# Optimization experiments

Hardware: AMD Instinct MI355X
Metric: run time of the kernel (lower is better)

The kernel has to match this reference:

```python
import jax, jax.numpy as jnp
import numpy as np
import math

D_MODEL = 1024
N_HEADS = 16
D_K = D_MODEL // N_HEADS


def setup_inputs() -> dict:
    key = jax.random.key(0)
    ks = jax.random.split(key, 9)
    s = 1.0 / math.sqrt(D_MODEL)
    x = jax.random.normal(ks[0], (2, 2048, D_MODEL), dtype=jnp.float32)
    # nn.Linear stores weight as [out, in]; we store transposed [in, out] for x @ W
    Wq = jax.random.uniform(ks[1], (D_MODEL, D_MODEL), jnp.float32, -s, s)
    bq = jax.random.uniform(ks[2], (D_MODEL,), jnp.float32, -s, s)
    Wk = jax.random.uniform(ks[3], (D_MODEL, D_MODEL), jnp.float32, -s, s)
    bk = jax.random.uniform(ks[4], (D_MODEL,), jnp.float32, -s, s)
    Wv = jax.random.uniform(ks[5], (D_MODEL, D_MODEL), jnp.float32, -s, s)
    bv = jax.random.uniform(ks[6], (D_MODEL,), jnp.float32, -s, s)
    Wo = jax.random.uniform(ks[7], (D_MODEL, D_MODEL), jnp.float32, -s, s)
    bo = jax.random.uniform(ks[8], (D_MODEL,), jnp.float32, -s, s)
    return {"x": x, "Wq": Wq, "bq": bq, "Wk": Wk, "bk": bk,
            "Wv": Wv, "bv": bv, "Wo": Wo, "bo": bo}


def reference(x, Wq, bq, Wk, bk, Wv, bv, Wo, bo):
    B, S, _ = x.shape
    scale = 1.0 / math.sqrt(D_K)
    # projections -> [B, H, S, Dk]
    def split_heads(t):
        return t.reshape(B, S, N_HEADS, D_K).transpose(0, 2, 1, 3)
    q = split_heads(x @ Wq + bq)
    k = split_heads(x @ Wk + bk)
    v = split_heads(x @ Wv + bv)
    # [B, H, S, S] scores
    scores = jnp.einsum('bhqd,bhkd->bhqk', q, k) * scale
    weights = jax.nn.softmax(scores, axis=-1)  # dropout p=0.0 -> identity
    attn = jnp.einsum('bhqk,bhkd->bhqd', weights, v)
    attn = attn.transpose(0, 2, 1, 3).reshape(B, S, D_MODEL)
    return attn @ Wo + bo
```

## Files before the change

### kernel.cpp

```cpp
#include <hip/hip_runtime.h>

#define DM    1024
#define NTOK  4096

typedef __attribute__((ext_vector_type(8))) short short8;
typedef __attribute__((ext_vector_type(4))) float floatx4;

__device__ __forceinline__ ushort f2bf(float f) {
  union { float f; uint32_t u; } v; v.f = f;
  uint32_t r = (v.u + 0x7fffu + ((v.u >> 16) & 1u)) >> 16;
  return (ushort)r;
}
__device__ __forceinline__ uint f2bf2(float a, float b) {
  return (uint)f2bf(a) | ((uint)f2bf(b) << 16);
}
__device__ __forceinline__ uint pkhi(float a, float b) {
  uint ua = __float_as_uint(a) + 0x8000u;
  uint ub = __float_as_uint(b) + 0x8000u;
  return __builtin_amdgcn_perm(ub, ua, 0x07060302);
}

__device__ __forceinline__ floatx4 mfma16(short8 a, short8 b, floatx4 c) {
  return __builtin_amdgcn_mfma_f32_16x16x32_bf16(a, b, c, 0, 0, 0);
}

__device__ __forceinline__ void glld16(const ushort* g, ushort* l) {
  __builtin_amdgcn_global_load_lds(
      (const __attribute__((address_space(1))) void*)g,
      (__attribute__((address_space(3))) void*)l, 16, 0, 0);
}

__device__ __forceinline__ void stage_slab(const ushort* gbase, int strideHW,
                                           ushort* lds, int ii, int lane) {
  const int r = ii * 8 + (lane >> 3);
  const int c = (lane & 7) ^ (r & 7);
  glld16(gbase + (size_t)r * strideHW + c * 8, lds + ii * 512);
}

__device__ __forceinline__ short8 fragr(const ushort* lds, int row, int chunk) {
  return *reinterpret_cast<const short8*>(&lds[row * 64 + ((chunk ^ (row & 7)) << 3)]);
}

__global__ __launch_bounds__(256) void k_prep(const float* __restrict__ x,
                                              const float* __restrict__ Wq,
                                              const float* __restrict__ Wk,
                                              const float* __restrict__ Wv,
                                              const float* __restrict__ Wo,
                                              ushort* __restrict__ xb,
                                              ushort* __restrict__ Wtout) {
  __shared__ ushort T[64 * 72];
  const int bx = blockIdx.x, tid = threadIdx.x;
  if (bx < 2048) {
    int i = (bx * 256 + tid) * 8;
    float4 f0 = *reinterpret_cast<const float4*>(x + i);
    float4 f1 = *reinterpret_cast<const float4*>(x + i + 4);
    short8 o;
    o[0] = (short)f2bf(f0.x); o[1] = (short)f2bf(f0.y);
    o[2] = (short)f2bf(f0.z); o[3] = (short)f2bf(f0.w);
    o[4] = (short)f2bf(f1.x); o[5] = (short)f2bf(f1.y);
    o[6] = (short)f2bf(f1.z); o[7] = (short)f2bf(f1.w);
    *reinterpret_cast<short8*>(xb + i) = o;
    return;
  }
  const int idx = bx - 2048;
  const int z = idx >> 8, rem = idx & 255;
  const float* W = (z == 0) ? Wq : (z == 1) ? Wk : (z == 2) ? Wv : Wo;
  ushort* Wt = Wtout + (size_t)z * (DM * DM);
  const int br = (rem >> 4) * 64;
  const int bc = (rem & 15) * 64;
  const int tr = tid >> 2;
  const int tc = (tid & 3) * 16;

  const float* src = W + (size_t)(br + tr) * DM + bc + tc;
#pragma unroll
  for (int j = 0; j < 4; ++j) {
    float4 v = *reinterpret_cast<const float4*>(src + j * 4);
    T[(tc + j * 4 + 0) * 72 + tr] = f2bf(v.x);
    T[(tc + j * 4 + 1) * 72 + tr] = f2bf(v.y);
    T[(tc + j * 4 + 2) * 72 + tr] = f2bf(v.z);
    T[(tc + j * 4 + 3) * 72 + tr] = f2bf(v.w);
  }
  __syncthreads();
  ushort* dst = Wt + (size_t)(bc + tr) * DM + br + tc;
  *reinterpret_cast<int4*>(dst) = *reinterpret_cast<const int4*>(&T[tr * 72 + tc]);
  *reinterpret_cast<int4*>(dst + 8) = *reinterpret_cast<const int4*>(&T[tr * 72 + tc + 8]);
}

__global__ __launch_bounds__(256) void k_gemm_qkv(const ushort* __restrict__ Am,
                                                  const ushort* __restrict__ Bm,
                                                  const float* __restrict__ bq,
                                                  const float* __restrict__ bk,
                                                  const float* __restrict__ bv,
                                                  ushort* __restrict__ Qo,
                                                  ushort* __restrict__ Ko,
                                                  ushort* __restrict__ Vto) {
  __shared__ ushort smem[32768];
  const int tid = threadIdx.x;
  const int w = tid >> 6, lane = tid & 63;
  const int quad = lane >> 4, l15 = lane & 15;
  const int wm = w >> 1, wn = w & 1;
  const int bm = blockIdx.x & 31, bn = blockIdx.x >> 5;
  const int sel = bn >> 3;
  const int bnl = bn & 7;

  const ushort* Ab = Am + (size_t)bm * 128 * 1024;
  const ushort* Bb = Bm + (size_t)bn * 128 * 1024;

  floatx4 acc[4][4] = {};

  auto stage = [&](int it, int buf) {
    ushort* As = smem + buf * 16384;
    ushort* Bs = As + 8192;
    const int k0 = it * 64;
#pragma unroll
    for (int i = 0; i < 4; ++i) stage_slab(Ab + k0, 1024, As, w * 4 + i, lane);
#pragma unroll
    for (int i = 0; i < 4; ++i) stage_slab(Bb + k0, 1024, Bs, w * 4 + i, lane);
  };

  stage(0, 0);
  for (int it = 0; it < 16; ++it) {
    __syncthreads();
    if (it + 1 < 16) stage(it + 1, (it + 1) & 1);
    const ushort* As = smem + (it & 1) * 16384;
    const ushort* Bs = As + 8192;
#pragma unroll
    for (int ks = 0; ks < 2; ++ks) {
      short8 af[4], bf[4];
#pragma unroll
      for (int t = 0; t < 4; ++t) {
        af[t] = fragr(As, wm * 64 + t * 16 + l15, ks * 4 + quad);
        bf[t] = fragr(Bs, wn * 64 + t * 16 + l15, ks * 4 + quad);
      }
#pragma unroll
      for (int tm = 0; tm < 4; ++tm)
#pragma unroll
        for (int tn = 0; tn < 4; ++tn)
          acc[tm][tn] = mfma16(af[tm], bf[tn], acc[tm][tn]);
    }
  }

  if (sel < 2) {
    const float* bp = sel ? bk : bq;
    ushort* dst = sel ? Ko : Qo;
    const float sc = sel ? 1.0f : 0.18033688f;
#pragma unroll
    for (int tm = 0; tm < 4; ++tm)
#pragma unroll
      for (int tn = 0; tn < 4; ++tn) {
        const int mg0 = bm * 128 + wm * 64 + tm * 16 + quad * 4;
        const int np = bnl * 128 + wn * 64 + tn * 16 + l15;
        const float bb = bp[np];
#pragma unroll
        for (int r = 0; r < 4; ++r) {
          const int m = mg0 + r;
          float v = (acc[tm][tn][r] + bb) * sc;
          dst[(size_t)((m >> 11) * 16 + (np >> 6)) * 131072 + (m & 2047) * 64 + (np & 63)] = f2bf(v);
        }
      }
  } else {
    __syncthreads();
    ushort* T = smem;
#pragma unroll
    for (int tm = 0; tm < 4; ++tm)
#pragma unroll
      for (int tn = 0; tn < 4; ++tn) {
        const int ml = wm * 64 + tm * 16 + quad * 4;
        const int nl = wn * 64 + tn * 16 + l15;
        const float bb = bv[bnl * 128 + nl];
        uint p0 = f2bf2(acc[tm][tn][0] + bb, acc[tm][tn][1] + bb);
        uint p1 = f2bf2(acc[tm][tn][2] + bb, acc[tm][tn][3] + bb);
        *reinterpret_cast<uint*>(&T[nl * 136 + ml]) = p0;
        *reinterpret_cast<uint*>(&T[nl * 136 + ml + 2]) = p1;
      }
    __syncthreads();
    const int tok0 = bm * 128;
    const int b = tok0 >> 11, s0 = tok0 & 2047;
    const int col = (tid & 15) * 8;
#pragma unroll
    for (int i = 0; i < 8; ++i) {
      const int rowl = i * 16 + (tid >> 4);
      const int dp = bnl * 128 + rowl;
      const int h = dp >> 6, d = dp & 63;
      *reinterpret_cast<int4*>(Vto + (size_t)((b * 16 + h) * 64 + d) * 2048 + s0 + col) =
          *reinterpret_cast<int4*>(&T[rowl * 136 + col]);
    }
  }
}

__global__ __launch_bounds__(256) void k_gemm_out(const ushort* __restrict__ Am,
                                                  const ushort* __restrict__ Bm,
                                                  const float* __restrict__ bias,
                                                  float* __restrict__ outp) {
  __shared__ ushort smem[24576];
  const int tid = threadIdx.x;
  const int w = tid >> 6, lane = tid & 63;
  const int quad = lane >> 4, l15 = lane & 15;
  const int wm = w >> 1, wn = w & 1;
  const int bm = blockIdx.x >> 3, bn = blockIdx.x & 7;

  const ushort* Ab = Am + (size_t)bm * 64 * 1024;
  const ushort* Bb = Bm + (size_t)bn * 128 * 1024;

  floatx4 acc[2][4] = {};

  auto stage = [&](int it, int buf) {
    ushort* As = smem + buf * 12288;
    ushort* Bs = As + 4096;
    const int k0 = it * 64;
#pragma unroll
    for (int i = 0; i < 2; ++i) stage_slab(Ab + k0, 1024, As, w * 2 + i, lane);
#pragma unroll
    for (int i = 0; i < 4; ++i) stage_slab(Bb + k0, 1024, Bs, w * 4 + i, lane);
  };

  stage(0, 0);
  for (int it = 0; it < 16; ++it) {
    __syncthreads();
    if (it + 1 < 16) stage(it + 1, (it + 1) & 1);
    const ushort* As = smem + (it & 1) * 12288;
    const ushort* Bs = As + 4096;
#pragma unroll
    for (int ks = 0; ks < 2; ++ks) {
      short8 af[2], bf[4];
#pragma unroll
      for (int t = 0; t < 2; ++t)
        af[t] = fragr(As, wm * 32 + t * 16 + l15, ks * 4 + quad);
#pragma unroll
      for (int t = 0; t < 4; ++t)
        bf[t] = fragr(Bs, wn * 64 + t * 16 + l15, ks * 4 + quad);
#pragma unroll
      for (int tm = 0; tm < 2; ++tm)
#pragma unroll
        for (int tn = 0; tn < 4; ++tn)
          acc[tm][tn] = mfma16(af[tm], bf[tn], acc[tm][tn]);
    }
  }

#pragma unroll
  for (int tm = 0; tm < 2; ++tm)
#pragma unroll
    for (int tn = 0; tn < 4; ++tn) {
      const int mg0 = bm * 64 + wm * 32 + tm * 16 + quad * 4;
      const int ng = bn * 128 + wn * 64 + tn * 16 + l15;
      const float bb = bias[ng];
#pragma unroll
      for (int r = 0; r < 4; ++r)
        outp[(size_t)(mg0 + r) * 1024 + ng] = acc[tm][tn][r] + bb;
    }
}

__global__ __launch_bounds__(256) void k_attn(const ushort* __restrict__ Q,
                                              const ushort* __restrict__ Kc,
                                              const ushort* __restrict__ Vt,
                                              ushort* __restrict__ attnb) {
  __shared__ ushort KV[2][16384];
  const int tid = threadIdx.x;
  const int w = tid >> 6, lane = tid & 63;
  const int quad = lane >> 4, l15 = lane & 15;
  const int bx = blockIdx.x;
  const int bh = (bx & 7) * 4 + ((bx >> 3) & 3);
  const int qc = bx >> 5;
  const int qt0 = qc * 128 + w * 32;
  const ushort* Qb = Q + (size_t)bh * 131072;
  const ushort* Kp = Kc + (size_t)bh * 131072;
  const ushort* Vp = Vt + (size_t)bh * 131072;

  short8 qf[2][2];
#pragma unroll
  for (int qs = 0; qs < 2; ++qs)
#pragma unroll
    for (int ks = 0; ks < 2; ++ks)
      qf[qs][ks] = *reinterpret_cast<const short8*>(
          Qb + (size_t)(qt0 + qs * 16 + l15) * 64 + ks * 32 + quad * 8);

  const int krho8 = lane >> 3;
  const int vt_ = (lane & 7) ^ (lane >> 3);

  auto stage = [&](int kt, int buf) {
#pragma unroll
    for (int i = 0; i < 2; ++i) {
      const int sub = (w & 1) * 2 + i;
      const int kc = kt * 128 + sub * 32;
      if (w < 2) {
        ushort* dst = &KV[buf][sub * 2048];
#pragma unroll
        for (int si = 0; si < 4; ++si) {
          const int rho = si * 8 + krho8;
          const int g = ((rho >> 2) & 3) * 8 + ((rho >> 4) & 1) * 4 + (rho & 3);
          const int cc = (lane & 7) ^ (rho & 7);
          glld16(Kp + (size_t)(kc + g) * 64 + cc * 8, dst + si * 512);
        }
      } else {
        ushort* dst = &KV[buf][8192 + sub * 2048];
#pragma unroll
        for (int si = 0; si < 4; ++si) {
          const int d = (si * 8 + krho8) * 2 + (vt_ >> 2);
          glld16(Vp + (size_t)d * 2048 + kc + (vt_ & 3) * 8, dst + si * 512);
        }
      }
    }
  };

  floatx4 oaccT[2][4] = {};
  floatx4 lacc[2] = {};

  auto computeChunk = [&](const ushort* Kb, const ushort* Vb) {
    floatx4 st[2][2] = {};
#pragma unroll
    for (int ks = 0; ks < 2; ++ks) {
      short8 kf0 = fragr(Kb, l15, ks * 4 + quad);
      short8 kf1 = fragr(Kb, 16 + l15, ks * 4 + quad);
      st[0][0] = mfma16(kf0, qf[0][ks], st[0][0]);
      st[0][1] = mfma16(kf1, qf[0][ks], st[0][1]);
      st[1][0] = mfma16(kf0, qf[1][ks], st[1][0]);
      st[1][1] = mfma16(kf1, qf[1][ks], st[1][1]);
    }
    short8 vf[4];
#pragma unroll
    for (int tn = 0; tn < 4; ++tn) {
      const int pg = tn * 8 + (l15 >> 1);
      const int cc = ((l15 & 1) * 4 + quad) ^ (l15 >> 1);
      vf[tn] = *reinterpret_cast<const short8*>(&Vb[pg * 64 + cc * 8]);
    }
#pragma unroll
    for (int qs = 0; qs < 2; ++qs) {
      floatx4 p0, p1;
#pragma unroll
      for (int r = 0; r < 4; ++r) {
        p0[r] = __builtin_amdgcn_exp2f(st[qs][0][r]);
        p1[r] = __builtin_amdgcn_exp2f(st[qs][1][r]);
      }
      lacc[qs] += p0;
      lacc[qs] += p1;
      union { uint4 u; short8 s; } pb;
      pb.u = (uint4){pkhi(p0[0], p0[1]), pkhi(p0[2], p0[3]),
                     pkhi(p1[0], p1[1]), pkhi(p1[2], p1[3])};
#pragma unroll
      for (int tn = 0; tn < 4; ++tn)
        oaccT[qs][tn] = mfma16(vf[tn], pb.s, oaccT[qs][tn]);
    }
  };

  stage(0, 0);
  for (int kt = 0; kt < 16; ++kt) {
    __syncthreads();
    if (kt + 1 < 16) stage(kt + 1, (kt + 1) & 1);
    const ushort* buf = KV[kt & 1];
#pragma unroll
    for (int c = 0; c < 4; ++c)
      computeChunk(buf + c * 2048, buf + 8192 + c * 2048);
  }

  float linv[2];
#pragma unroll
  for (int qs = 0; qs < 2; ++qs) {
    float l = lacc[qs][0] + lacc[qs][1] + lacc[qs][2] + lacc[qs][3];
    l += __shfl_xor(l, 16);
    l += __shfl_xor(l, 32);
    linv[qs] = 1.0f / l;
  }

  const int b = bh >> 4, h = bh & 15;
#pragma unroll
  for (int qs = 0; qs < 2; ++qs) {
    const int tok = b * 2048 + qt0 + qs * 16 + l15;
#pragma unroll
    for (int tn = 0; tn < 4; ++tn) {
      float v0 = oaccT[qs][tn][0] * linv[qs];
      float v1 = oaccT[qs][tn][1] * linv[qs];
      float v2 = oaccT[qs][tn][2] * linv[qs];
      float v3 = oaccT[qs][tn][3] * linv[qs];
      ushort* p = attnb + (size_t)tok * 1024 + h * 64 + tn * 16 + quad * 4;
      *reinterpret_cast<uint*>(p) = pkhi(v0, v1);
      *reinterpret_cast<uint*>(p + 2) = pkhi(v2, v3);
    }
  }
}

extern "C" void kernel_launch(void* const* d_in, const int* in_sizes, int n_in,
                              void* d_out, int out_size, void* d_ws, size_t ws_size,
                              hipStream_t stream) {
  const float* x  = (const float*)d_in[0];
  const float* Wq = (const float*)d_in[1];
  const float* bq = (const float*)d_in[2];
  const float* Wk = (const float*)d_in[3];
  const float* bk = (const float*)d_in[4];
  const float* Wv = (const float*)d_in[5];
  const float* bv = (const float*)d_in[6];
  const float* Wo = (const float*)d_in[7];
  const float* bo = (const float*)d_in[8];

  ushort* ws = (ushort*)d_ws;
  ushort* xb    = ws;
  ushort* Wqt   = ws + 4194304;
  ushort* Wot   = ws + 7340032;
  ushort* Qb    = ws + 8388608;
  ushort* Kbuf  = ws + 12582912;
  ushort* Vtb   = ws + 16777216;
  ushort* attnb = ws + 20971520;

  k_prep<<<3072, 256, 0, stream>>>(x, Wq, Wk, Wv, Wo, xb, Wqt);
  k_gemm_qkv<<<768, 256, 0, stream>>>(xb, Wqt, bq, bk, bv, Qb, Kbuf, Vtb);
  k_attn<<<512, 256, 0, stream>>>(Qb, Kbuf, Vtb, attnb);
  k_gemm_out<<<512, 256, 0, stream>>>(attnb, Wot, bo, (float*)d_out);
}
```

Baseline: 183.6 us.

## Halve attention KV tile, compute softmax denominator via MFMA, use packed bf16 convert

The attention kernel's shared K/V staging buffer is halved (64 keys per stage instead of 128), doubling the loop count while cutting LDS per block, which may allow more resident blocks. The per-lane fp32 row-sum accumulation and cross-lane shuffles are replaced by an extra MFMA against a vector of bf16 ones, so the denominator comes out of the matrix unit. The probability packing uses the hardware cvt_pk_bf16 instruction when available. The trade-off is more barriers and stage iterations, an extra MFMA per chunk, and a denominator summed from bf16-rounded probabilities.

```diff
diff --git a/kernel.cpp b/kernel.cpp
--- a/kernel.cpp
+++ b/kernel.cpp
@@ -5,6 +5,7 @@
 
 typedef __attribute__((ext_vector_type(8))) short short8;
 typedef __attribute__((ext_vector_type(4))) float floatx4;
+typedef __attribute__((ext_vector_type(2))) __bf16 bf16x2;
 
 __device__ __forceinline__ ushort f2bf(float f) {
   union { float f; uint32_t u; } v; v.f = f;
@@ -18,6 +19,15 @@
   uint ua = __float_as_uint(a) + 0x8000u;
   uint ub = __float_as_uint(b) + 0x8000u;
   return __builtin_amdgcn_perm(ub, ua, 0x07060302);
+}
+__device__ __forceinline__ uint pk2(float a, float b) {
+#if __has_builtin(__builtin_amdgcn_cvt_pk_bf16_f32)
+  bf16x2 v = __builtin_amdgcn_cvt_pk_bf16_f32(a, b);
+  union { bf16x2 v; uint u; } c; c.v = v;
+  return c.u;
+#else
+  return pkhi(a, b);
+#endif
 }
 
 __device__ __forceinline__ floatx4 mfma16(short8 a, short8 b, floatx4 c) {
@@ -254,7 +264,7 @@
                                               const ushort* __restrict__ Kc,
                                               const ushort* __restrict__ Vt,
                                               ushort* __restrict__ attnb) {
-  __shared__ ushort KV[2][16384];
+  __shared__ ushort KV[2][8192];
   const int tid = threadIdx.x;
   const int w = tid >> 6, lane = tid & 63;
   const int quad = lane >> 4, l15 = lane & 15;
@@ -274,36 +284,36 @@
       qf[qs][ks] = *reinterpret_cast<const short8*>(
           Qb + (size_t)(qt0 + qs * 16 + l15) * 64 + ks * 32 + quad * 8);
 
+  short8 ones;
+#pragma unroll
+  for (int i = 0; i < 8; ++i) ones[i] = (short)0x3F80;
+
   const int krho8 = lane >> 3;
   const int vt_ = (lane & 7) ^ (lane >> 3);
 
   auto stage = [&](int kt, int buf) {
-#pragma unroll
-    for (int i = 0; i < 2; ++i) {
-      const int sub = (w & 1) * 2 + i;
-      const int kc = kt * 128 + sub * 32;
-      if (w < 2) {
-        ushort* dst = &KV[buf][sub * 2048];
-#pragma unroll
-        for (int si = 0; si < 4; ++si) {
-          const int rho = si * 8 + krho8;
-          const int g = ((rho >> 2) & 3) * 8 + ((rho >> 4) & 1) * 4 + (rho & 3);
-          const int cc = (lane & 7) ^ (rho & 7);
-          glld16(Kp + (size_t)(kc + g) * 64 + cc * 8, dst + si * 512);
-        }
-      } else {
-        ushort* dst = &KV[buf][8192 + sub * 2048];
-#pragma unroll
-        for (int si = 0; si < 4; ++si) {
-          const int d = (si * 8 + krho8) * 2 + (vt_ >> 2);
-          glld16(Vp + (size_t)d * 2048 + kc + (vt_ & 3) * 8, dst + si * 512);
-        }
+    const int c = w & 1;
+    ushort* dst = &KV[buf][(w >> 1) * 4096 + c * 2048];
+    const int kc = kt * 64 + c * 32;
+    if (w < 2) {
+#pragma unroll
+      for (int si = 0; si < 4; ++si) {
+        const int rho = si * 8 + krho8;
+        const int g = ((rho >> 2) & 3) * 8 + ((rho >> 4) & 1) * 4 + (rho & 3);
+        const int cc = (lane & 7) ^ (rho & 7);
+        glld16(Kp + (size_t)(kc + g) * 64 + cc * 8, dst + si * 512);
+      }
+    } else {
+#pragma unroll
+      for (int si = 0; si < 4; ++si) {
+        const int d = (si * 8 + krho8) * 2 + (vt_ >> 2);
+        glld16(Vp + (size_t)d * 2048 + kc + (vt_ & 3) * 8, dst + si * 512);
       }
     }
   };
 
   floatx4 oaccT[2][4] = {};
-  floatx4 lacc[2] = {};
+  floatx4 oaccL[2] = {};
 
   auto computeChunk = [&](const ushort* Kb, const ushort* Vb) {
     floatx4 st[2][2] = {};
@@ -331,35 +341,28 @@
         p0[r] = __builtin_amdgcn_exp2f(st[qs][0][r]);
         p1[r] = __builtin_amdgcn_exp2f(st[qs][1][r]);
       }
-      lacc[qs] += p0;
-      lacc[qs] += p1;
       union { uint4 u; short8 s; } pb;
-      pb.u = (uint4){pkhi(p0[0], p0[1]), pkhi(p0[2], p0[3]),
-                     pkhi(p1[0], p1[1]), pkhi(p1[2], p1[3])};
+      pb.u = (uint4){pk2(p0[0], p0[1]), pk2(p0[2], p0[3]),
+                     pk2(p1[0], p1[1]), pk2(p1[2], p1[3])};
 #pragma unroll
       for (int tn = 0; tn < 4; ++tn)
         oaccT[qs][tn] = mfma16(vf[tn], pb.s, oaccT[qs][tn]);
+      oaccL[qs] = mfma16(ones, pb.s, oaccL[qs]);
     }
   };
 
   stage(0, 0);
-  for (int kt = 0; kt < 16; ++kt) {
+  for (int kt = 0; kt < 32; ++kt) {
     __syncthreads();
-    if (kt + 1 < 16) stage(kt + 1, (kt + 1) & 1);
+    if (kt + 1 < 32) stage(kt + 1, (kt + 1) & 1);
     const ushort* buf = KV[kt & 1];
-#pragma unroll
-    for (int c = 0; c < 4; ++c)
-      computeChunk(buf + c * 2048, buf + 8192 + c * 2048);
+    computeChunk(buf, buf + 4096);
+    computeChunk(buf + 2048, buf + 6144);
   }
 
   float linv[2];
 #pragma unroll
-  for (int qs = 0; qs < 2; ++qs) {
-    float l = lacc[qs][0] + lacc[qs][1] + lacc[qs][2] + lacc[qs][3];
-    l += __shfl_xor(l, 16);
-    l += __shfl_xor(l, 32);
-    linv[qs] = 1.0f / l;
-  }
+  for (int qs = 0; qs < 2; ++qs) linv[qs] = 1.0f / oaccL[qs][0];
 
   const int b = bh >> 4, h = bh & 15;
 #pragma unroll
```

Result: no change. 184.9 us, median of 2 (+0.7%).
